# Performance work log

Hardware: AMD Instinct MI355X
Metric: run time of the kernel (lower is better)

Reference implementation:

```python
import jax, jax.numpy as jnp
from jax import lax
import numpy as np

IN_C = 256
PREV_IN_C = 256
OUT_C = 128
ATTN = IN_C // 8  # attn_size == attn_out == 32


def setup_inputs() -> dict:
    key = jax.random.key(0)
    ks = jax.random.split(key, 12)
    B, W, H = 4, 64, 64
    s = 0.02
    return {
        "source_enc_f": jax.random.normal(ks[0], (B, IN_C, W, H), jnp.float32),
        "target_enc_f": jax.random.normal(ks[1], (B, IN_C, W, H), jnp.float32),
        "prev_inp": jax.random.normal(ks[2], (B, PREV_IN_C, W // 2, H // 2), jnp.float32),
        "key_w": s * jax.random.normal(ks[3], (ATTN, IN_C), jnp.float32),
        "key_b": jnp.zeros((ATTN,), jnp.float32),
        "query_w": s * jax.random.normal(ks[4], (ATTN, IN_C), jnp.float32),
        "query_b": jnp.zeros((ATTN,), jnp.float32),
        "lin_w": s * jax.random.normal(ks[5], (ATTN, 2 * ATTN), jnp.float32),  # k_q_linear: cat([key, query])
        "lin_b": jnp.zeros((ATTN,), jnp.float32),
        "attn_w": s * jax.random.normal(ks[6], (IN_C, ATTN + IN_C), jnp.float32),
        "attn_b": jnp.zeros((IN_C,), jnp.float32),
        "gamma": jnp.array(0.1, jnp.float32),  # torch inits 0.0; nonzero so attn path is exercised
        "conv_w": s * jax.random.normal(ks[7], (OUT_C, IN_C + PREV_IN_C, 3, 3), jnp.float32),
        "conv_b": jnp.zeros((OUT_C,), jnp.float32),
    }


def _forward(source_enc_f, target_enc_f, prev_inp, key_w, key_b, query_w, query_b,
             lin_w, lin_b, attn_w, attn_b, gamma, conv_w, conv_b):
    B, C, W, H = source_enc_f.shape
    WH = W * H
    A = ATTN
    # 1x1 convs for query/key
    q = jnp.einsum('oc,bchw->bohw', query_w, source_enc_f) + query_b[:, None, None]
    k = jnp.einsum('oc,bchw->bohw', key_w, target_enc_f) + key_b[:, None, None]
    # Original: for every (key pos a, query pos c) pair, Linear(cat(key[a], query[c])),
    # then sum over c. Linear is separable: out[a] = WH*(Wk@key[a] + b) + Wq @ sum_c query[c].
    Wk, Wq = lin_w[:, :A], lin_w[:, A:]
    key_term = jnp.einsum('oa,bahw->bohw', Wk, k)          # [B, attn_out, W, H]
    q_sum = jnp.einsum('oa,ba->bo', Wq, q.sum(axis=(2, 3)))  # [B, attn_out]
    attn_map = WH * (key_term + lin_b[:, None, None]) + q_sum[:, :, None, None]
    # attn_conv (1x1) over cat([target, attn_map])
    x = jnp.concatenate([target_enc_f, attn_map], axis=1)
    out = jnp.einsum('oc,bchw->bohw', attn_w, x) + attn_b[:, None, None]
    x = target_enc_f + gamma * out
    prev_up = jnp.repeat(jnp.repeat(prev_inp, 2, axis=2), 2, axis=3)
    x = jnp.concatenate([x, prev_up], axis=1)
    y = lax.conv_general_dilated(x, conv_w, (1, 1), 'SAME',
                                 dimension_numbers=('NCHW', 'OIHW', 'NCHW'))
    y = y + conv_b[:, None, None]
    mean = y.mean(axis=(2, 3), keepdims=True)
    var = y.var(axis=(2, 3), keepdims=True)  # biased, as torch InstanceNorm2d
    y = (y - mean) * lax.rsqrt(var + 1e-5)
    return jax.nn.relu(y)


def reference(source_enc_f, target_enc_f, prev_inp, key_w, key_b, query_w, query_b,
              lin_w, lin_b, attn_w, attn_b, gamma, conv_w, conv_b):
    return _forward(source_enc_f, target_enc_f, prev_inp, key_w, key_b, query_w, query_b,
                    lin_w, lin_b, attn_w, attn_b, gamma, conv_w, conv_b)
```

## Files before the change

### kernel.cpp

```cpp
#include <hip/hip_runtime.h>

typedef unsigned short u16;
typedef __attribute__((ext_vector_type(8))) __bf16 bf16x8;
typedef __attribute__((ext_vector_type(8))) unsigned short u16x8;
typedef __attribute__((ext_vector_type(4))) float f32x4;

__device__ __forceinline__ u16 f2bf(float f) {
  unsigned u = __builtin_bit_cast(unsigned, f);
  unsigned r = u + 0x7fffu + ((u >> 16) & 1u);
  return (u16)(r >> 16);
}

__device__ __forceinline__ float wave_sum(float v) {
#pragma unroll
  for (int o = 32; o; o >>= 1) v += __shfl_xor(v, o, 64);
  return v;
}

__device__ __forceinline__ void gl2lds16(const u16* g, u16* l) {
  __builtin_amdgcn_global_load_lds(
      (const __attribute__((address_space(1))) unsigned int*)(const void*)g,
      (__attribute__((address_space(3))) unsigned int*)(void*)l, 16, 0, 0);
}

__global__ void k0(const float* __restrict__ src, const float* __restrict__ kw,
                   const float* __restrict__ lw, const float* __restrict__ aw,
                   const float* __restrict__ gamma,
                   float* __restrict__ ssum, float* __restrict__ Mt) {
  __shared__ float red[64];
  int tid = threadIdx.x;
  if (blockIdx.x >= 1024) {
    int o = blockIdx.x - 1024;
    if (tid < 32) {
      float s = 0.f;
      for (int o2 = 0; o2 < 32; ++o2) s += aw[o * 288 + 256 + o2] * lw[o2 * 64 + tid];
      red[tid] = s;
    }
    __syncthreads();
    float s = 0.f;
    for (int a = 0; a < 32; ++a) s += red[a] * kw[a * 256 + tid];
    Mt[o * 256 + tid] = gamma[0] * (aw[o * 288 + tid] + 4096.f * s) + (o == tid ? 1.f : 0.f);
    return;
  }
  int plane = blockIdx.x;
  const float* p = src + (size_t)plane * 4096;
  float s = 0.f;
#pragma unroll
  for (int i = 0; i < 4; ++i) {
    f32x4 v = *(const f32x4*)(p + (i * 256 + tid) * 4);
    s += v[0] + v[1] + v[2] + v[3];
  }
  s = wave_sum(s);
  if ((tid & 63) == 0) red[tid >> 6] = s;
  __syncthreads();
  if (tid == 0) ssum[plane] = red[0] + red[1] + red[2] + red[3];
}

__global__ void k1(const float* __restrict__ tgt, const float* __restrict__ prev,
                   const float* __restrict__ cw, const float* __restrict__ Mt,
                   const float* __restrict__ ssum,
                   const float* __restrict__ qw, const float* __restrict__ qb,
                   const float* __restrict__ kb, const float* __restrict__ lw,
                   const float* __restrict__ lb, const float* __restrict__ aw,
                   const float* __restrict__ ab, const float* __restrict__ gamma,
                   u16* __restrict__ xin, u16* __restrict__ w3,
                   float* __restrict__ cd2) {
  int tid = threadIdx.x;
  if (blockIdx.x >= 256) {
    __shared__ float qs_l[128], amap_l[128], dvec_l[1024];
    __shared__ float cwl[4096];
    __shared__ float part[512];
    if (tid < 128) {
      int bb = tid >> 5, o = tid & 31;
      float s = 4096.f * qb[o];
      for (int c = 0; c < 256; ++c) s += qw[o * 256 + c] * ssum[bb * 256 + c];
      qs_l[tid] = s;
    }
    __syncthreads();
    if (tid < 128) {
      int bb = tid >> 5, o2 = tid & 31;
      float s = 0.f, kt = 0.f;
      for (int o = 0; o < 32; ++o) {
        s += lw[o2 * 64 + 32 + o] * qs_l[bb * 32 + o];
        kt += lw[o2 * 64 + o] * kb[o];
      }
      amap_l[tid] = 4096.f * (kt + lb[o2]) + s;
    }
    __syncthreads();
    float g = gamma[0];
    for (int i = tid; i < 1024; i += 512) {
      int bb = i >> 8, c = i & 255;
      float s = ab[c];
      for (int o2 = 0; o2 < 32; ++o2) s += aw[c * 288 + 256 + o2] * amap_l[bb * 32 + o2];
      dvec_l[i] = g * s;
    }
    int blk = blockIdx.x - 256;
    int tap = blk >> 4, ocg = blk & 15;
    for (int e = tid; e < 4096; e += 512) {
      int oc = e >> 9, c = e & 511;
      cwl[e] = cw[(size_t)((ocg * 8 + oc) * 512 + c) * 9 + tap];
    }
    __syncthreads();
    int wv = tid >> 6, l = tid & 63;
    int c2 = l * 4;
    f32x4 acc = {0.f, 0.f, 0.f, 0.f};
    for (int c = 0; c < 256; ++c) {
      float wc = cwl[wv * 512 + c];
      f32x4 m = *(const f32x4*)(Mt + c * 256 + c2);
#pragma unroll
      for (int j = 0; j < 4; ++j) acc[j] += wc * m[j];
    }
    int ocf = ocg * 8 + wv;
#pragma unroll
    for (int j2 = 0; j2 < 4; ++j2) {
      int cf = c2 + j2;
      w3[(tap * 16 + (cf >> 5)) * 4096 + ((cf >> 3) & 3) * 1024 + ocf * 8 + (cf & 7)] = f2bf(acc[j2]);
      cf = 256 + c2 + j2;
      w3[(tap * 16 + (cf >> 5)) * 4096 + ((cf >> 3) & 3) * 1024 + ocf * 8 + (cf & 7)] =
          f2bf(cwl[wv * 512 + (c2 + j2 + 256)]);
    }
    {
      int bb = tid >> 7, oc = (tid >> 4) & 7, cp = tid & 15;
      float s = 0.f;
#pragma unroll
      for (int i = 0; i < 16; ++i) s += cwl[oc * 512 + cp * 16 + i] * dvec_l[bb * 256 + cp * 16 + i];
      part[tid] = s;
    }
    __syncthreads();
    if (tid < 32) {
      int bb = tid >> 3, oc = tid & 7;
      float s = 0.f;
#pragma unroll
      for (int cp = 0; cp < 16; ++cp) s += part[bb * 128 + oc * 16 + cp];
      cd2[(size_t)(bb * 128 + ocg * 8 + oc) * 9 + tap] = s;
    }
    return;
  }
  __shared__ u16 lt[16896];
  int b = blockIdx.x >> 6, h = blockIdx.x & 63;
  u16* slab = xin + (size_t)(b * 64 + h) * 40960;
  if (tid < 256) {
    int cg = tid >> 4, colidx = tid & 15;
    int pxp = (colidx == 0) ? 0 : (64 + colidx);
    u16x8 zz;
#pragma unroll
    for (int q = 0; q < 8; ++q) zz[q] = 0;
    u16* d = slab + cg * 2560 + pxp * 32;
    *(u16x8*)(d) = zz; *(u16x8*)(d + 8) = zz;
    *(u16x8*)(d + 16) = zz; *(u16x8*)(d + 24) = zz;
  }
#pragma unroll
  for (int it = 0; it < 8; ++it) {
    int fi = it * 512 + tid;
    int c = fi >> 4, w4 = fi & 15;
    f32x4 v = *(const f32x4*)(tgt + ((size_t)(b * 256 + c) * 64 + h) * 64 + w4 * 4);
    int base = c * 66 + w4 * 4;
    lt[base] = f2bf(v[0]); lt[base + 1] = f2bf(v[1]);
    lt[base + 2] = f2bf(v[2]); lt[base + 3] = f2bf(v[3]);
  }
  __syncthreads();
  {
    int cg = tid >> 6, l = tid & 63;
    int s = l & 3;
#pragma unroll
    for (int it = 0; it < 4; ++it) {
      int pxp = 1 + it * 16 + (l >> 2);
      int g = s ^ ((pxp >> 1) & 3);
      int o = cg * 4 + g;
      int w = pxp - 1;
      u16x8 v;
#pragma unroll
      for (int k = 0; k < 8; ++k) v[k] = lt[(o * 8 + k) * 66 + w];
      *(u16x8*)(slab + cg * 2560 + pxp * 32 + s * 8) = v;
    }
  }
  __syncthreads();
#pragma unroll
  for (int it = 0; it < 4; ++it) {
    int pi = it * 512 + tid;
    int cc = pi >> 3, wq = pi & 7;
    f32x4 v = *(const f32x4*)(prev + ((size_t)(b * 256 + cc) * 32 + (h >> 1)) * 32 + wq * 4);
    int base = cc * 66 + wq * 8;
    u16 b0 = f2bf(v[0]), b1 = f2bf(v[1]), b2 = f2bf(v[2]), b3 = f2bf(v[3]);
    lt[base] = b0; lt[base + 1] = b0; lt[base + 2] = b1; lt[base + 3] = b1;
    lt[base + 4] = b2; lt[base + 5] = b2; lt[base + 6] = b3; lt[base + 7] = b3;
  }
  __syncthreads();
  {
    int cg8 = tid >> 6, l = tid & 63;
    int s = l & 3;
#pragma unroll
    for (int it = 0; it < 4; ++it) {
      int pxp = 1 + it * 16 + (l >> 2);
      int g = s ^ ((pxp >> 1) & 3);
      int o = cg8 * 4 + g;
      int w = pxp - 1;
      u16x8 v;
#pragma unroll
      for (int k = 0; k < 8; ++k) v[k] = lt[(o * 8 + k) * 66 + w];
      *(u16x8*)(slab + (8 + cg8) * 2560 + pxp * 32 + s * 8) = v;
    }
  }
}

__global__ __launch_bounds__(512) void k_conv(const u16* __restrict__ xin,
                                              const u16* __restrict__ w3,
                                              const float* __restrict__ cd2,
                                              float* __restrict__ out) {
  __shared__ u16 lds[52736];
  const int XIN0 = 36864, DUMMY = 52224;
  int bid = blockIdx.x;
  int lid = (bid & 7) * 32 + (bid >> 3);
  int b = lid >> 6, h = lid & 63;
  int tid = threadIdx.x, l = tid & 63, wv = tid >> 6;
  int wr = wv & 3, wpx = wv >> 2;
  int r = l & 15, kb4 = l >> 4;

  if (h == 0 || h == 63) {
    int row = (h == 0) ? 0 : 2;
    for (int i = tid; i < 640; i += 512) {
      int bu = i / 320, off = (i % 320) * 8;
      u16x8 zz;
#pragma unroll
      for (int q = 0; q < 8; ++q) zz[q] = 0;
      *(u16x8*)(lds + XIN0 + bu * 7680 + row * 2560 + off) = zz;
    }
  }

  auto ISSUE_W3 = [&](int c2, int dy2, int buf, bool dummy) {
    u16* dst0 = lds + buf * 12288;
#pragma unroll
    for (int i = 0; i < 3; ++i) {
      int k = wv + 8 * i;
      int dx = k >> 3, part = k & 7;
      const u16* src = dummy ? (w3 + l * 8)
          : (w3 + (size_t)(((dy2 * 3 + dx) * 16 + c2) << 12) + part * 512 + l * 8);
      u16* dst = dummy ? (lds + DUMMY) : (dst0 + dx * 4096 + part * 512);
      gl2lds16(src, dst);
    }
  };
  auto ISSUE_XIN = [&](int c1, int buf, bool dummyAll) {
    u16* dst0 = lds + XIN0 + buf * 7680;
#pragma unroll
    for (int i = 0; i < 2; ++i) {
      int k = wv + 8 * i;
      int row = k / 5, part = k - row * 5;
      int grow = h - 1 + row;
      bool dm = dummyAll || (k == 15) || ((unsigned)grow >= 64u);
      const u16* src = dm ? (xin + l * 8)
          : (xin + ((size_t)(b * 64 + grow) * 16 + c1) * 2560 + part * 512 + l * 8);
      u16* dst = dm ? (lds + DUMMY) : (dst0 + row * 2560 + part * 512);
      gl2lds16(src, dst);
    }
  };

  f32x4 acc[2][2];
#pragma unroll
  for (int mf = 0; mf < 2; ++mf)
#pragma unroll
    for (int nf = 0; nf < 2; ++nf) acc[mf][nf] = f32x4{0.f, 0.f, 0.f, 0.f};

  ISSUE_W3(0, 0, 0, false);
  ISSUE_XIN(0, 0, false);
  ISSUE_W3(0, 1, 1, false);

  for (int c = 0; c < 16; ++c) {
#pragma unroll
    for (int dy = 0; dy < 3; ++dy) {
      if (dy == 0) asm volatile("s_waitcnt vmcnt(3) lgkmcnt(0)" ::: "memory");
      else         asm volatile("s_waitcnt vmcnt(5) lgkmcnt(0)" ::: "memory");
      __builtin_amdgcn_s_barrier();
      __builtin_amdgcn_sched_barrier(0);
      {
        int c2 = c + ((dy + 2) / 3);
        ISSUE_W3(c2, (dy + 2) % 3, (dy + 2) % 3, c2 > 15);
      }
      if (dy == 0) ISSUE_XIN(c + 1, (c + 1) & 1, c + 1 > 15);
      const u16* wbuf = lds + dy * 12288;
      const u16* xrow = lds + XIN0 + (c & 1) * 7680 + dy * 2560;
#pragma unroll
      for (int dx = 0; dx < 3; ++dx) {
        bf16x8 av[2];
#pragma unroll
        for (int mf = 0; mf < 2; ++mf)
          av[mf] = *(const bf16x8*)(wbuf + dx * 4096 + kb4 * 1024 + (wr * 32 + mf * 16 + r) * 8);
        bf16x8 bv[2];
#pragma unroll
        for (int nf = 0; nf < 2; ++nf) {
          int pxp = wpx * 32 + nf * 16 + r + dx;
          int slot = kb4 ^ ((pxp >> 1) & 3);
          bv[nf] = *(const bf16x8*)(xrow + pxp * 32 + slot * 8);
        }
#pragma unroll
        for (int mf = 0; mf < 2; ++mf)
#pragma unroll
          for (int nf = 0; nf < 2; ++nf)
            acc[mf][nf] = __builtin_amdgcn_mfma_f32_16x16x32_bf16(av[mf], bv[nf], acc[mf][nf], 0, 0, 0);
      }
    }
  }

  bool dy0v = (h > 0), dy2v = (h < 63);
#pragma unroll
  for (int mf = 0; mf < 2; ++mf) {
#pragma unroll
    for (int j = 0; j < 4; ++j) {
      int oc = wr * 32 + mf * 16 + kb4 * 4 + j;
      const float* cd = cd2 + (size_t)(b * 128 + oc) * 9;
      float sAll = 0.f, sL = 0.f, sR = 0.f;
#pragma unroll
      for (int dy3 = 0; dy3 < 3; ++dy3) {
        bool v = (dy3 == 1) || (dy3 == 0 ? dy0v : dy2v);
        if (v) {
          sAll += cd[dy3 * 3] + cd[dy3 * 3 + 1] + cd[dy3 * 3 + 2];
          sL += cd[dy3 * 3];
          sR += cd[dy3 * 3 + 2];
        }
      }
#pragma unroll
      for (int nf = 0; nf < 2; ++nf) {
        int px = wpx * 32 + nf * 16 + r;
        float corr = sAll - (px == 0 ? sL : 0.f) - (px == 63 ? sR : 0.f);
        out[(size_t)(b * 128 + oc) * 4096 + h * 64 + px] = acc[mf][nf][j] + corr;
      }
    }
  }
}

__global__ void k_norm(float* __restrict__ out) {
  int plane = blockIdx.x;
  float* p = out + (size_t)plane * 4096;
  int t = threadIdx.x;
  f32x4 v[4];
  float s = 0.f, s2 = 0.f;
#pragma unroll
  for (int i = 0; i < 4; ++i) {
    v[i] = *(const f32x4*)(p + (i * 256 + t) * 4);
#pragma unroll
    for (int k = 0; k < 4; ++k) { s += v[i][k]; s2 += v[i][k] * v[i][k]; }
  }
  s = wave_sum(s); s2 = wave_sum(s2);
  __shared__ float rs[4], rs2[4];
  if ((t & 63) == 0) { rs[t >> 6] = s; rs2[t >> 6] = s2; }
  __syncthreads();
  float S = rs[0] + rs[1] + rs[2] + rs[3];
  float S2 = rs2[0] + rs2[1] + rs2[2] + rs2[3];
  float mean = S * (1.f / 4096.f);
  float var = S2 * (1.f / 4096.f) - mean * mean;
  float inv = rsqrtf(var + 1e-5f);
#pragma unroll
  for (int i = 0; i < 4; ++i) {
    f32x4 o;
#pragma unroll
    for (int k = 0; k < 4; ++k) {
      float y = (v[i][k] - mean) * inv;
      o[k] = y > 0.f ? y : 0.f;
    }
    *(f32x4*)(p + (i * 256 + t) * 4) = o;
  }
}

extern "C" void kernel_launch(void* const* d_in, const int* in_sizes, int n_in,
                              void* d_out, int out_size, void* d_ws, size_t ws_size,
                              hipStream_t stream) {
  const float* src    = (const float*)d_in[0];
  const float* tgt    = (const float*)d_in[1];
  const float* prev   = (const float*)d_in[2];
  const float* key_w  = (const float*)d_in[3];
  const float* key_b  = (const float*)d_in[4];
  const float* qry_w  = (const float*)d_in[5];
  const float* qry_b  = (const float*)d_in[6];
  const float* lin_w  = (const float*)d_in[7];
  const float* lin_b  = (const float*)d_in[8];
  const float* attn_w = (const float*)d_in[9];
  const float* attn_b = (const float*)d_in[10];
  const float* gamma  = (const float*)d_in[11];
  const float* conv_w = (const float*)d_in[12];

  char* ws = (char*)d_ws;
  size_t off = 0;
  u16*   xin  = (u16*)(ws + off);  off += 20971520;
  float* ssum = (float*)(ws + off); off += 4096;
  float* Mt   = (float*)(ws + off); off += 262144;
  float* cd2  = (float*)(ws + off); off += 18432;
  u16*   w3   = (u16*)(ws + off);  off += 1179648;
  float* out  = (float*)d_out;

  k0<<<1280, 256, 0, stream>>>(src, key_w, lin_w, attn_w, gamma, ssum, Mt);
  k1<<<400, 512, 0, stream>>>(tgt, prev, conv_w, Mt, ssum, qry_w, qry_b, key_b,
                              lin_w, lin_b, attn_w, attn_b, gamma, xin, w3, cd2);
  k_conv<<<256, 512, 0, stream>>>(xin, w3, cd2, out);
  k_norm<<<512, 256, 0, stream>>>(out);
}
```

Before: 71.88 us.

## Split per-batch attention bias chain into dedicated blocks and unify shared memory

Previously each of the 144 weight-folding blocks redundantly computed the whole query/attn_map/dvec chain for all batches before doing its tap work. Now four extra blocks, one per batch, compute that chain once with a parallelised query reduction and write cd2 directly. The weight-folding blocks only fold weights, with an unrolled inner loop. Shared memory is merged into one aliased buffer so k1's per-block LDS footprint shrinks. The catch is that cd2 is now computed by a strided global read of conv_w in only four blocks, which may become a tail.

```diff
diff --git a/kernel.cpp b/kernel.cpp
--- a/kernel.cpp
+++ b/kernel.cpp
@@ -65,35 +65,64 @@
                    const float* __restrict__ ab, const float* __restrict__ gamma,
                    u16* __restrict__ xin, u16* __restrict__ w3,
                    float* __restrict__ cd2) {
+  __shared__ __align__(16) unsigned char smem[33792];
   int tid = threadIdx.x;
+  if (blockIdx.x >= 400) {
+    float* S = (float*)smem;
+    float* part = S;
+    float* qs = S + 512;
+    float* amap = S + 544;
+    float* dvec = S + 576;
+    int b = blockIdx.x - 400;
+    {
+      int o = tid >> 4, seg = tid & 15;
+      float s = 0.f;
+#pragma unroll
+      for (int i = 0; i < 8; ++i) {
+        int c = seg * 16 + i * 2;
+        s += qw[o * 256 + c] * ssum[b * 256 + c];
+        s += qw[o * 256 + c + 1] * ssum[b * 256 + c + 1];
+      }
+      part[tid] = s;
+    }
+    __syncthreads();
+    if (tid < 32) {
+      float s = 4096.f * qb[tid];
+#pragma unroll
+      for (int k = 0; k < 16; ++k) s += part[tid * 16 + k];
+      qs[tid] = s;
+    }
+    __syncthreads();
+    if (tid < 32) {
+      int o2 = tid;
+      float s = 0.f, kt = 0.f;
+#pragma unroll 8
+      for (int o = 0; o < 32; ++o) {
+        s += lw[o2 * 64 + 32 + o] * qs[o];
+        kt += lw[o2 * 64 + o] * kb[o];
+      }
+      amap[o2] = 4096.f * (kt + lb[o2]) + s;
+    }
+    __syncthreads();
+    if (tid < 256) {
+      float g = gamma[0];
+      float s = ab[tid];
+#pragma unroll 8
+      for (int o2 = 0; o2 < 32; ++o2) s += aw[tid * 288 + 256 + o2] * amap[o2];
+      dvec[tid] = g * s;
+    }
+    __syncthreads();
+    for (int p = tid; p < 1152; p += 512) {
+      int oc = p / 9, tap = p - oc * 9;
+      float s = 0.f;
+#pragma unroll 8
+      for (int c = 0; c < 256; ++c) s += cw[(size_t)(oc * 512 + c) * 9 + tap] * dvec[c];
+      cd2[(size_t)(b * 128 + oc) * 9 + tap] = s;
+    }
+    return;
+  }
   if (blockIdx.x >= 256) {
-    __shared__ float qs_l[128], amap_l[128], dvec_l[1024];
-    __shared__ float cwl[4096];
-    __shared__ float part[512];
-    if (tid < 128) {
-      int bb = tid >> 5, o = tid & 31;
-      float s = 4096.f * qb[o];
-      for (int c = 0; c < 256; ++c) s += qw[o * 256 + c] * ssum[bb * 256 + c];
-      qs_l[tid] = s;
-    }
-    __syncthreads();
-    if (tid < 128) {
-      int bb = tid >> 5, o2 = tid & 31;
-      float s = 0.f, kt = 0.f;
-      for (int o = 0; o < 32; ++o) {
-        s += lw[o2 * 64 + 32 + o] * qs_l[bb * 32 + o];
-        kt += lw[o2 * 64 + o] * kb[o];
-      }
-      amap_l[tid] = 4096.f * (kt + lb[o2]) + s;
-    }
-    __syncthreads();
-    float g = gamma[0];
-    for (int i = tid; i < 1024; i += 512) {
-      int bb = i >> 8, c = i & 255;
-      float s = ab[c];
-      for (int o2 = 0; o2 < 32; ++o2) s += aw[c * 288 + 256 + o2] * amap_l[bb * 32 + o2];
-      dvec_l[i] = g * s;
-    }
+    float* cwl = (float*)smem;
     int blk = blockIdx.x - 256;
     int tap = blk >> 4, ocg = blk & 15;
     for (int e = tid; e < 4096; e += 512) {
@@ -104,6 +133,7 @@
     int wv = tid >> 6, l = tid & 63;
     int c2 = l * 4;
     f32x4 acc = {0.f, 0.f, 0.f, 0.f};
+#pragma unroll 8
     for (int c = 0; c < 256; ++c) {
       float wc = cwl[wv * 512 + c];
       f32x4 m = *(const f32x4*)(Mt + c * 256 + c2);
@@ -119,24 +149,9 @@
       w3[(tap * 16 + (cf >> 5)) * 4096 + ((cf >> 3) & 3) * 1024 + ocf * 8 + (cf & 7)] =
           f2bf(cwl[wv * 512 + (c2 + j2 + 256)]);
     }
-    {
-      int bb = tid >> 7, oc = (tid >> 4) & 7, cp = tid & 15;
-      float s = 0.f;
-#pragma unroll
-      for (int i = 0; i < 16; ++i) s += cwl[oc * 512 + cp * 16 + i] * dvec_l[bb * 256 + cp * 16 + i];
-      part[tid] = s;
-    }
-    __syncthreads();
-    if (tid < 32) {
-      int bb = tid >> 3, oc = tid & 7;
-      float s = 0.f;
-#pragma unroll
-      for (int cp = 0; cp < 16; ++cp) s += part[bb * 128 + oc * 16 + cp];
-      cd2[(size_t)(bb * 128 + ocg * 8 + oc) * 9 + tap] = s;
-    }
     return;
   }
-  __shared__ u16 lt[16896];
+  u16* lt = (u16*)smem;
   int b = blockIdx.x >> 6, h = blockIdx.x & 63;
   u16* slab = xin + (size_t)(b * 64 + h) * 40960;
   if (tid < 256) {
@@ -387,7 +402,7 @@
   float* out  = (float*)d_out;
 
   k0<<<1280, 256, 0, stream>>>(src, key_w, lin_w, attn_w, gamma, ssum, Mt);
-  k1<<<400, 512, 0, stream>>>(tgt, prev, conv_w, Mt, ssum, qry_w, qry_b, key_b,
+  k1<<<404, 512, 0, stream>>>(tgt, prev, conv_w, Mt, ssum, qry_w, qry_b, key_b,
                               lin_w, lin_b, attn_w, attn_b, gamma, xin, w3, cd2);
   k_conv<<<256, 512, 0, stream>>>(xin, w3, cd2, out);
   k_norm<<<512, 256, 0, stream>>>(out);
```

Result: slower. 105.6 us (+47.0%).
